# Kernel optimization log

Measured on AMD Instinct MI355X. Metric: run time of the kernel, lower is better.

The kernel has to match this reference:

```python
import jax, jax.numpy as jnp
import numpy as np

N_NODES = 50000
N_EDGES = 800000
NEG_SLOPE = 0.2  # PyG GATv2Conv default
EPS = 1e-16      # PyG softmax denominator epsilon


def _segment_softmax(logits, seg, num_segments):
    # logits: [E, H]; seg: [E] target-node ids
    m = jax.ops.segment_max(logits, seg, num_segments=num_segments)
    p = jnp.exp(logits - m[seg])
    s = jax.ops.segment_sum(p, seg, num_segments=num_segments)
    return p / (s[seg] + EPS)


def _gatv2_conv(x, src, dst, Wl, Wr, att, bias, heads, out_ch, concat):
    # x: [N, F]; Wl/Wr: [F, heads*out_ch]; att: [heads, out_ch]
    n = x.shape[0]
    xl = (x @ Wl).reshape(n, heads, out_ch)
    xr = (x @ Wr).reshape(n, heads, out_ch)
    # GATv2: e_ij = att . leaky_relu(xl[j] + xr[i]) for edge j->i
    e = jax.nn.leaky_relu(xl[src] + xr[dst], NEG_SLOPE)  # [E, H, C]
    logit = jnp.einsum('ehc,hc->eh', e, att)             # [E, H]
    alpha = _segment_softmax(logit, dst, n)              # [E, H]
    out = jax.ops.segment_sum(alpha[:, :, None] * xl[src], dst, num_segments=n)  # [N, H, C]
    if concat:
        out = out.reshape(n, heads * out_ch)
    else:
        out = out.mean(axis=1)
    return out + bias


def setup_inputs() -> dict:
    key = jax.random.key(0)
    ks = jax.random.split(key, 20)
    in_ch, hid, out_ch, heads, edge_dim = 128, 128, 64, 8, 6
    c1 = hid // heads  # 16
    g = lambda k, shp, fan: (jax.random.normal(k, shp, jnp.float32) / np.sqrt(fan)).astype(jnp.float32)
    inp = {
        'x': jax.random.normal(ks[0], (N_NODES, in_ch), jnp.float32),
        'edge_index': jax.random.randint(ks[1], (2, N_EDGES), 0, N_NODES, dtype=jnp.int64),
        'edge_attr': jax.random.normal(ks[2], (N_EDGES, edge_dim), jnp.float32),
        'Wl1': g(ks[3], (in_ch, heads * c1), in_ch),
        'Wr1': g(ks[4], (in_ch, heads * c1), in_ch),
        'att1': g(ks[5], (heads, c1), c1),
        'b1': jnp.zeros((heads * c1,), jnp.float32),
        # layer 2: GATv2Conv(hid -> out_ch, heads=1, no concat)
        'Wl2': g(ks[6], (hid, out_ch), hid),
        'Wr2': g(ks[7], (hid, out_ch), hid),
        'att2': g(ks[8], (1, out_ch), out_ch),
        'b2': jnp.zeros((out_ch,), jnp.float32),
        # edge encoder (computed but unused downstream, as in the source)
        'We1': g(ks[9], (edge_dim, hid), edge_dim), 'be1': jnp.zeros((hid,), jnp.float32),
        'We2': g(ks[10], (hid, hid), hid), 'be2': jnp.zeros((hid,), jnp.float32),
        # classifier
        'Wc1': g(ks[11], (out_ch, hid), out_ch), 'bc1': jnp.zeros((hid,), jnp.float32),
        'Wc2': g(ks[12], (hid, 2), hid), 'bc2': jnp.zeros((2,), jnp.float32),
    }
    return inp


def reference(x, edge_index, edge_attr, Wl1, Wr1, att1, b1, Wl2, Wr2, att2, b2,
              We1, be1, We2, be2, Wc1, bc1, Wc2, bc2):
    n = x.shape[0]
    # edge encoder (dead code in the original forward; kept for fidelity)
    _edge_feats = jax.nn.relu(edge_attr @ We1 + be1) @ We2 + be2
    # add self-loops (PyG GATv2Conv default add_self_loops=True)
    loop = jnp.arange(n, dtype=edge_index.dtype)
    src = jnp.concatenate([edge_index[0], loop])
    dst = jnp.concatenate([edge_index[1], loop])
    # layer 1 (heads=8, concat) + relu; dropout is identity in eval
    h = _gatv2_conv(x, src, dst, Wl1, Wr1, att1, b1, heads=8, out_ch=16, concat=True)
    h = jax.nn.relu(h)
    # layer 2 (heads=1, mean)
    emb = _gatv2_conv(h, src, dst, Wl2, Wr2, att2, b2, heads=1, out_ch=64, concat=False)
    logits = jax.nn.relu(emb @ Wc1 + bc1) @ Wc2 + bc2
    return emb, logits
```

## Files before the change

kernel.cpp:

```cpp
#include <hip/hip_runtime.h>
#include <hip/hip_bf16.h>
#include <cfloat>

#define N_NODES 50000
#define N_EDGES 800000
#define E_TOT   850000
#define NEG_SLOPE 0.2f
#define SM_EPS 1e-16f
#define SCAN_B 196
#define LOG2E 1.4426950408889634f

typedef __attribute__((ext_vector_type(8))) short short8;
typedef __attribute__((ext_vector_type(4))) float f32x4;

__device__ __forceinline__ float lrelu(float v) { return v > 0.0f ? v : NEG_SLOPE * v; }

__device__ __forceinline__ unsigned f2bf_pack2(float a, float b) {
    unsigned ua = __float_as_uint(a);
    ua += 0x7fff + ((ua >> 16) & 1);
    unsigned ub = __float_as_uint(b);
    ub += 0x7fff + ((ub >> 16) & 1);
    return (ua >> 16) | (ub & 0xffff0000u);
}
__device__ __forceinline__ unsigned short f2bf(float a) {
    unsigned ua = __float_as_uint(a);
    ua += 0x7fff + ((ua >> 16) & 1);
    return (unsigned short)(ua >> 16);
}
__device__ __forceinline__ float bf_lo(unsigned u) { return __uint_as_float(u << 16); }
__device__ __forceinline__ float bf_hi(unsigned u) { return __uint_as_float(u & 0xffff0000u); }

__device__ __forceinline__ unsigned short pack_one(const float* __restrict__ B0,
                                                   const float* __restrict__ B1,
                                                   int i, int N) {
    int m   = i / (128 * N);
    int rem = i % (128 * N);
    int j    = rem & 7;
    int quad = (rem >> 3) & 3;
    int n    = (rem >> 5) & 15;
    int ctk  = rem >> 9;
    int ct   = ctk % (N / 16);
    int kt   = ctk / (N / 16);
    int k    = kt * 32 + quad * 8 + j;
    int col  = ct * 16 + n;
    const float* B = m ? B1 : B0;
    return f2bf(B[k * N + col]);
}

__global__ void prep(const float* __restrict__ Wl1, const float* __restrict__ Wr1,
                     const float* __restrict__ Wl2, const float* __restrict__ Wr2,
                     const float* __restrict__ Wc1,
                     unsigned short* __restrict__ Bp1, unsigned short* __restrict__ Bp2,
                     unsigned short* __restrict__ Wc1p,
                     int* __restrict__ flags) {
    int i = blockIdx.x * 256 + threadIdx.x;
    if (i < 32768) {
        Bp1[i] = pack_one(Wl1, Wr1, i, 128);
    } else if (i < 49152) {
        Bp2[i - 32768] = pack_one(Wl2, Wr2, i - 32768, 64);
    } else if (i < 57344) {
        int idx = i - 49152;
        int j    = idx & 7;
        int quad = (idx >> 3) & 3;
        int n    = (idx >> 5) & 15;
        int ctk  = idx >> 9;
        int ct   = ctk & 7;
        int kt   = ctk >> 3;
        Wc1p[idx] = f2bf(Wc1[(kt * 32 + quad * 8 + j) * 128 + ct * 16 + n]);
    } else if (i < 57600) {
        flags[i - 57344] = 0;
    }
}

__device__ __forceinline__ void gemm128_both(int b, const float* __restrict__ x,
                                             const unsigned short* __restrict__ Bp1,
                                             unsigned short* __restrict__ xlbf,
                                             float* __restrict__ xr1, int M) {
    int w = threadIdx.x >> 6, lane = threadIdx.x & 63;
    int quad = lane >> 4, l16 = lane & 15;
    int row0 = b * 32 + (w & 1) * 16;
    int cb   = (w >> 1) * 64;
    f32x4 accL[4], accR[4];
    #pragma unroll
    for (int t = 0; t < 4; ++t) {
        accL[t] = (f32x4){0.f, 0.f, 0.f, 0.f};
        accR[t] = (f32x4){0.f, 0.f, 0.f, 0.f};
    }
    int arow = row0 + l16;
    bool aok = arow < M;
    #pragma unroll
    for (int kt = 0; kt < 4; ++kt) {
        short8 a = (short8)0;
        if (aok) {
            const float* Ap = x + (size_t)arow * 128 + quad * 8 + kt * 32;
            float4 f0 = *(const float4*)(Ap);
            float4 f1 = *(const float4*)(Ap + 4);
            union { uint4 u; short8 s; } cv;
            cv.u.x = f2bf_pack2(f0.x, f0.y);
            cv.u.y = f2bf_pack2(f0.z, f0.w);
            cv.u.z = f2bf_pack2(f1.x, f1.y);
            cv.u.w = f2bf_pack2(f1.z, f1.w);
            a = cv.s;
        }
        #pragma unroll
        for (int t = 0; t < 4; ++t) {
            int ct = (cb >> 4) + t;
            const short* bp = (const short*)Bp1 + (((kt * 8 + ct) * 16 + l16) * 4 + quad) * 8;
            short8 bL = *(const short8*)bp;
            short8 bR = *(const short8*)(bp + 128 * 128);
            accL[t] = __builtin_amdgcn_mfma_f32_16x16x32_bf16(a, bL, accL[t], 0, 0, 0);
            accR[t] = __builtin_amdgcn_mfma_f32_16x16x32_bf16(a, bR, accR[t], 0, 0, 0);
        }
    }
    #pragma unroll
    for (int t = 0; t < 4; ++t) {
        int col = cb + t * 16 + l16;
        #pragma unroll
        for (int r = 0; r < 4; ++r) {
            int row = row0 + quad * 4 + r;
            if (row < M) {
                xlbf[(size_t)row * 128 + col] = f2bf(accL[t][r]);
                xr1[(size_t)row * 128 + col]  = accR[t][r];
            }
        }
    }
}

__global__ __launch_bounds__(256)
void k2_count_gemms(const int* __restrict__ ei, unsigned* __restrict__ deg8,
                    unsigned short* __restrict__ rank16,
                    const float* __restrict__ x, const unsigned short* __restrict__ Bp1,
                    unsigned short* __restrict__ xlbf, float* __restrict__ xr1, int M) {
    int b = blockIdx.x;
    int c = b / 3, rem = b % 3;
    if (rem == 2) {
        int nz = __syncthreads_or(ei[2 * threadIdx.x + 1]);
        int i = c * 256 + threadIdx.x;
        if (4 * i >= N_EDGES) return;
        int d0, d1, d2, d3;
        if (nz) {
            int4 dp = *(const int4*)(ei + N_EDGES + 4 * i);
            d0 = dp.x; d1 = dp.y; d2 = dp.z; d3 = dp.w;
        } else {
            int4 a0 = *(const int4*)(ei + 2 * N_EDGES + 8 * i);
            int4 a1 = *(const int4*)(ei + 2 * N_EDGES + 8 * i + 4);
            d0 = a0.x; d1 = a0.z; d2 = a1.x; d3 = a1.z;
        }
        unsigned xcd;
        asm volatile("s_getreg_b32 %0, hwreg(HW_REG_XCC_ID)" : "=s"(xcd));
        xcd &= 7u;
        unsigned* dg = deg8 + xcd * 50000u;
        unsigned tag = xcd << 13;
        unsigned r0 = __hip_atomic_fetch_add(&dg[d0], 1u, __ATOMIC_RELAXED, __HIP_MEMORY_SCOPE_WORKGROUP);
        unsigned r1 = __hip_atomic_fetch_add(&dg[d1], 1u, __ATOMIC_RELAXED, __HIP_MEMORY_SCOPE_WORKGROUP);
        unsigned r2 = __hip_atomic_fetch_add(&dg[d2], 1u, __ATOMIC_RELAXED, __HIP_MEMORY_SCOPE_WORKGROUP);
        unsigned r3 = __hip_atomic_fetch_add(&dg[d3], 1u, __ATOMIC_RELAXED, __HIP_MEMORY_SCOPE_WORKGROUP);
        uint2 pk;
        pk.x = (r0 | tag) | ((r1 | tag) << 16);
        pk.y = (r2 | tag) | ((r3 | tag) << 16);
        *(uint2*)(rank16 + 4 * i) = pk;
    } else {
        int g = 2 * c + rem;
        if (g >= 1563) return;
        gemm128_both(g, x, Bp1, xlbf, xr1, M);
    }
}

__global__ void scan_fused(const unsigned* __restrict__ deg8, int* __restrict__ rowptr,
                           int* __restrict__ esrc, int* __restrict__ bsum,
                           int* __restrict__ flags, int* __restrict__ base8) {
    __shared__ int sh[256];
    int b = blockIdx.x, t = threadIdx.x, i = b * 256 + t;
    unsigned d[8];
    int tot = 0;
    if (i < N_NODES) {
        #pragma unroll
        for (int xk = 0; xk < 8; ++xk) { d[xk] = deg8[xk * 50000 + i]; tot += (int)d[xk]; }
    }
    int v = (i < N_NODES) ? tot + 1 : 0;
    sh[t] = v;
    __syncthreads();
    int val = v;
    for (int off = 1; off < 256; off <<= 1) {
        int add = (t >= off) ? sh[t - off] : 0;
        __syncthreads();
        val += add; sh[t] = val;
        __syncthreads();
    }
    if (t == 255) {
        bsum[b] = val;
        __threadfence();
        atomicExch(&flags[b], 1);
    }
    int contrib = 0;
    if (t < b) {
        while (atomicAdd(&flags[t], 0) == 0) {}
        contrib = atomicAdd(&bsum[t], 0);
    }
    __syncthreads();
    sh[t] = contrib;
    __syncthreads();
    #pragma unroll
    for (int off = 128; off; off >>= 1) {
        if (t < off) sh[t] += sh[t + off];
        __syncthreads();
    }
    int offset = sh[0];
    if (i < N_NODES) {
        int rp = (val - v) + offset;
        rowptr[i] = rp;
        esrc[rp] = i;
        int acc = rp + 1;
        #pragma unroll
        for (int xk = 0; xk < 8; ++xk) { base8[xk * 50000 + i] = acc; acc += (int)d[xk]; }
    }
    if (i == 0) rowptr[N_NODES] = E_TOT;
}

__global__ void scatter_edges(const int* __restrict__ ei, const int* __restrict__ base8,
                              const unsigned short* __restrict__ rank16,
                              int* __restrict__ esrc) {
    int nz = __syncthreads_or(ei[2 * threadIdx.x + 1]);
    int i = blockIdx.x * blockDim.x + threadIdx.x;
    if (2 * i >= N_EDGES) return;
    bool has2 = (2 * i + 1 < N_EDGES);
    int s0, d0, s1 = 0, d1 = 0;
    if (nz) {
        int2 sp = *(const int2*)(ei + 2 * i);
        int2 dp = *(const int2*)(ei + N_EDGES + 2 * i);
        s0 = sp.x; s1 = sp.y; d0 = dp.x; d1 = dp.y;
    } else {
        int4 sp = *(const int4*)(ei + 4 * i);
        int4 dp = *(const int4*)(ei + 2 * N_EDGES + 4 * i);
        s0 = sp.x; s1 = sp.z; d0 = dp.x; d1 = dp.z;
    }
    unsigned rr = *(const unsigned*)(rank16 + 2 * i);
    unsigned r0 = rr & 0xffffu, r1 = rr >> 16;
    esrc[base8[(r0 >> 13) * 50000 + d0] + (int)(r0 & 0x1fffu)] = s0;
    if (has2) esrc[base8[(r1 >> 13) * 50000 + d1] + (int)(r1 & 0x1fffu)] = s1;
}

__global__ __launch_bounds__(256)
void gemm_mfma64(const unsigned short* __restrict__ Abf, const unsigned short* __restrict__ Bp,
                 unsigned short* __restrict__ C0bf, float* __restrict__ C1, int M) {
    int w = threadIdx.x >> 6, lane = threadIdx.x & 63;
    int quad = lane >> 4, l16 = lane & 15;
    int matrix = w >> 1;
    int row0 = blockIdx.x * 32 + (w & 1) * 16;
    const unsigned short* Bm = Bp + matrix * 128 * 64;
    f32x4 acc[4];
    #pragma unroll
    for (int t = 0; t < 4; ++t) acc[t] = (f32x4){0.f, 0.f, 0.f, 0.f};
    int arow = row0 + l16;
    bool aok = arow < M;
    const short* Ap = (const short*)Abf + (size_t)arow * 128 + quad * 8;
    #pragma unroll
    for (int kt = 0; kt < 4; ++kt) {
        short8 a = (short8)0;
        if (aok) a = *(const short8*)(Ap + kt * 32);
        #pragma unroll
        for (int t = 0; t < 4; ++t) {
            const short* bp = (const short*)Bm + (((kt * 4 + t) * 16 + l16) * 4 + quad) * 8;
            short8 bfr = *(const short8*)bp;
            acc[t] = __builtin_amdgcn_mfma_f32_16x16x32_bf16(a, bfr, acc[t], 0, 0, 0);
        }
    }
    #pragma unroll
    for (int t = 0; t < 4; ++t) {
        int col = t * 16 + l16;
        #pragma unroll
        for (int r = 0; r < 4; ++r) {
            int row = row0 + quad * 4 + r;
            if (row < M) {
                if (matrix) C1[(size_t)row * 64 + col] = acc[t][r];
                else        C0bf[(size_t)row * 64 + col] = f2bf(acc[t][r]);
            }
        }
    }
}

__global__ __launch_bounds__(256)
void node_fused1(const int* __restrict__ rowptr, const int* __restrict__ esrc,
                 const unsigned short* __restrict__ xlbf, const float* __restrict__ xr,
                 const float* __restrict__ att, const float* __restrict__ b1,
                 unsigned short* __restrict__ hbf) {
    int wave = threadIdx.x >> 6;
    int lane = threadIdx.x & 63;
    int n = blockIdx.x * 4 + wave;
    int slot = lane >> 4;
    int l = lane & 15;
    int beg = rowptr[n], end = rowptr[n + 1];
    const float* xrp = xr + (size_t)n * 128 + 8 * l;
    float4 xra = *(const float4*)(xrp);
    float4 xrb = *(const float4*)(xrp + 4);
    float4 ata = *(const float4*)(att + 8 * l);
    float4 atb = *(const float4*)(att + 8 * l + 4);
    ata.x *= LOG2E; ata.y *= LOG2E; ata.z *= LOG2E; ata.w *= LOG2E;
    atb.x *= LOG2E; atb.y *= LOG2E; atb.z *= LOG2E; atb.w *= LOG2E;
    float den = 0.0f;
    float4 aa = {0, 0, 0, 0}, ab = {0, 0, 0, 0};

    auto body = [&](int k) {
        int s = esrc[k];
        uint4 u = *(const uint4*)(xlbf + (size_t)s * 128 + 8 * l);
        float x0 = bf_lo(u.x), x1 = bf_hi(u.x);
        float x2 = bf_lo(u.y), x3 = bf_hi(u.y);
        float x4 = bf_lo(u.z), x5 = bf_hi(u.z);
        float x6 = bf_lo(u.w), x7 = bf_hi(u.w);
        float v = ata.x * lrelu(x0 + xra.x) + ata.y * lrelu(x1 + xra.y)
                + ata.z * lrelu(x2 + xra.z) + ata.w * lrelu(x3 + xra.w)
                + atb.x * lrelu(x4 + xrb.x) + atb.y * lrelu(x5 + xrb.y)
                + atb.z * lrelu(x6 + xrb.z) + atb.w * lrelu(x7 + xrb.w);
        v += __shfl_xor(v, 1);
        float p = exp2f(v);
        den += p;
        aa.x += p * x0; aa.y += p * x1; aa.z += p * x2; aa.w += p * x3;
        ab.x += p * x4; ab.y += p * x5; ab.z += p * x6; ab.w += p * x7;
    };
    int k = beg + slot;
    for (; k + 4 < end; k += 8) { body(k); body(k + 4); }
    if (k < end) body(k);

    #pragma unroll
    for (int off = 16; off < 64; off <<= 1) {
        aa.x += __shfl_xor(aa.x, off); aa.y += __shfl_xor(aa.y, off);
        aa.z += __shfl_xor(aa.z, off); aa.w += __shfl_xor(aa.w, off);
        ab.x += __shfl_xor(ab.x, off); ab.y += __shfl_xor(ab.y, off);
        ab.z += __shfl_xor(ab.z, off); ab.w += __shfl_xor(ab.w, off);
        den   += __shfl_xor(den, off);
    }
    if (slot == 0) {
        float inv = 1.0f / (den + SM_EPS);
        float4 b4a = *(const float4*)(b1 + 8 * l);
        float4 b4b = *(const float4*)(b1 + 8 * l + 4);
        float oa0 = fmaxf(aa.x * inv + b4a.x, 0.0f);
        float oa1 = fmaxf(aa.y * inv + b4a.y, 0.0f);
        float oa2 = fmaxf(aa.z * inv + b4a.z, 0.0f);
        float oa3 = fmaxf(aa.w * inv + b4a.w, 0.0f);
        float ob0 = fmaxf(ab.x * inv + b4b.x, 0.0f);
        float ob1 = fmaxf(ab.y * inv + b4b.y, 0.0f);
        float ob2 = fmaxf(ab.z * inv + b4b.z, 0.0f);
        float ob3 = fmaxf(ab.w * inv + b4b.w, 0.0f);
        uint4 pk;
        pk.x = f2bf_pack2(oa0, oa1);
        pk.y = f2bf_pack2(oa2, oa3);
        pk.z = f2bf_pack2(ob0, ob1);
        pk.w = f2bf_pack2(ob2, ob3);
        *(uint4*)(hbf + (size_t)n * 128 + 8 * l) = pk;
    }
}

__global__ __launch_bounds__(256)
void node_fused2(const int* __restrict__ rowptr, const int* __restrict__ esrc,
                 const unsigned short* __restrict__ xlbf, const float* __restrict__ xr,
                 const float* __restrict__ att, const float* __restrict__ b2v,
                 float* __restrict__ out_emb, unsigned short* __restrict__ embbf) {
    int wave = threadIdx.x >> 6;
    int lane = threadIdx.x & 63;
    int n = blockIdx.x * 4 + wave;
    int slot = lane >> 3;
    int l = lane & 7;
    int beg = rowptr[n], end = rowptr[n + 1];
    const float* xrp = xr + (size_t)n * 64 + 8 * l;
    float4 xra = *(const float4*)(xrp);
    float4 xrb = *(const float4*)(xrp + 4);
    float4 ata = *(const float4*)(att + 8 * l);
    float4 atb = *(const float4*)(att + 8 * l + 4);
    ata.x *= LOG2E; ata.y *= LOG2E; ata.z *= LOG2E; ata.w *= LOG2E;
    atb.x *= LOG2E; atb.y *= LOG2E; atb.z *= LOG2E; atb.w *= LOG2E;
    float den = 0.0f;
    float4 aa = {0, 0, 0, 0}, ab = {0, 0, 0, 0};

    auto body = [&](int k) {
        int s = esrc[k];
        uint4 u = *(const uint4*)(xlbf + (size_t)s * 64 + 8 * l);
        float x0 = bf_lo(u.x), x1 = bf_hi(u.x);
        float x2 = bf_lo(u.y), x3 = bf_hi(u.y);
        float x4 = bf_lo(u.z), x5 = bf_hi(u.z);
        float x6 = bf_lo(u.w), x7 = bf_hi(u.w);
        float v = ata.x * lrelu(x0 + xra.x) + ata.y * lrelu(x1 + xra.y)
                + ata.z * lrelu(x2 + xra.z) + ata.w * lrelu(x3 + xra.w)
                + atb.x * lrelu(x4 + xrb.x) + atb.y * lrelu(x5 + xrb.y)
                + atb.z * lrelu(x6 + xrb.z) + atb.w * lrelu(x7 + xrb.w);
        v += __shfl_xor(v, 1);
        v += __shfl_xor(v, 2);
        v += __shfl_xor(v, 4);
        float p = exp2f(v);
        den += p;
        aa.x += p * x0; aa.y += p * x1; aa.z += p * x2; aa.w += p * x3;
        ab.x += p * x4; ab.y += p * x5; ab.z += p * x6; ab.w += p * x7;
    };
    int k = beg + slot;
    for (; k + 8 < end; k += 16) { body(k); body(k + 8); }
    if (k < end) body(k);

    #pragma unroll
    for (int off = 8; off < 64; off <<= 1) {
        aa.x += __shfl_xor(aa.x, off); aa.y += __shfl_xor(aa.y, off);
        aa.z += __shfl_xor(aa.z, off); aa.w += __shfl_xor(aa.w, off);
        ab.x += __shfl_xor(ab.x, off); ab.y += __shfl_xor(ab.y, off);
        ab.z += __shfl_xor(ab.z, off); ab.w += __shfl_xor(ab.w, off);
        den   += __shfl_xor(den, off);
    }
    if (slot == 0) {
        float inv = 1.0f / (den + SM_EPS);
        float4 b4a = *(const float4*)(b2v + 8 * l);
        float4 b4b = *(const float4*)(b2v + 8 * l + 4);
        float4 ea, eb;
        ea.x = aa.x * inv + b4a.x; ea.y = aa.y * inv + b4a.y;
        ea.z = aa.z * inv + b4a.z; ea.w = aa.w * inv + b4a.w;
        eb.x = ab.x * inv + b4b.x; eb.y = ab.y * inv + b4b.y;
        eb.z = ab.z * inv + b4b.z; eb.w = ab.w * inv + b4b.w;
        float* op = out_emb + (size_t)n * 64 + 8 * l;
        *(float4*)(op)     = ea;
        *(float4*)(op + 4) = eb;
        uint4 pk;
        pk.x = f2bf_pack2(ea.x, ea.y);
        pk.y = f2bf_pack2(ea.z, ea.w);
        pk.z = f2bf_pack2(eb.x, eb.y);
        pk.w = f2bf_pack2(eb.z, eb.w);
        *(uint4*)(embbf + (size_t)n * 64 + 8 * l) = pk;
    }
}

__global__ __launch_bounds__(256)
void cls_mfma(const unsigned short* __restrict__ embbf, const unsigned short* __restrict__ Wc1p,
              const float* __restrict__ bc1, const float* __restrict__ Wc2,
              const float* __restrict__ bc2, float* __restrict__ out_logits) {
    __shared__ float part[2][16][2][2];
    int w = threadIdx.x >> 6, lane = threadIdx.x & 63;
    int quad = lane >> 4, l16 = lane & 15;
    int rowhalf = w & 1, colhalf = w >> 1;
    int row0 = blockIdx.x * 32 + rowhalf * 16;
    int cb = colhalf * 64;
    f32x4 acc[4];
    #pragma unroll
    for (int t = 0; t < 4; ++t) acc[t] = (f32x4){0.f, 0.f, 0.f, 0.f};
    int arow = row0 + l16;
    bool aok = arow < N_NODES;
    const short* Ap = (const short*)embbf + (size_t)arow * 64 + quad * 8;
    #pragma unroll
    for (int kt = 0; kt < 2; ++kt) {
        short8 a = (short8)0;
        if (aok) a = *(const short8*)(Ap + kt * 32);
        #pragma unroll
        for (int t = 0; t < 4; ++t) {
            int ct = colhalf * 4 + t;
            const short* bp = (const short*)Wc1p + (((kt * 8 + ct) * 16 + l16) * 4 + quad) * 8;
            short8 bfr = *(const short8*)bp;
            acc[t] = __builtin_amdgcn_mfma_f32_16x16x32_bf16(a, bfr, acc[t], 0, 0, 0);
        }
    }
    float p0[4] = {0, 0, 0, 0}, p1[4] = {0, 0, 0, 0};
    #pragma unroll
    for (int t = 0; t < 4; ++t) {
        int col = cb + t * 16 + l16;
        float w2a = Wc2[2 * col], w2b = Wc2[2 * col + 1];
        float bc = bc1[col];
        #pragma unroll
        for (int r = 0; r < 4; ++r) {
            float tv = fmaxf(acc[t][r] + bc, 0.0f);
            p0[r] += tv * w2a;
            p1[r] += tv * w2b;
        }
    }
    #pragma unroll
    for (int off = 1; off < 16; off <<= 1) {
        #pragma unroll
        for (int r = 0; r < 4; ++r) {
            p0[r] += __shfl_xor(p0[r], off);
            p1[r] += __shfl_xor(p1[r], off);
        }
    }
    if (l16 == 0) {
        #pragma unroll
        for (int r = 0; r < 4; ++r) {
            part[rowhalf][quad * 4 + r][colhalf][0] = p0[r];
            part[rowhalf][quad * 4 + r][colhalf][1] = p1[r];
        }
    }
    __syncthreads();
    int t = threadIdx.x;
    if (t < 64) {
        int row = t >> 1, c = t & 1;
        int rh = row >> 4, r16 = row & 15;
        float s = part[rh][r16][0][c] + part[rh][r16][1][c] + bc2[c];
        int n = blockIdx.x * 32 + row;
        if (n < N_NODES) out_logits[(size_t)n * 2 + c] = s;
    }
}

extern "C" void kernel_launch(void* const* d_in, const int* in_sizes, int n_in,
                              void* d_out, int out_size, void* d_ws, size_t ws_size,
                              hipStream_t stream) {
    const float* x    = (const float*)d_in[0];
    const int*   ei   = (const int*)d_in[1];
    const float* Wl1  = (const float*)d_in[3];
    const float* Wr1  = (const float*)d_in[4];
    const float* att1 = (const float*)d_in[5];
    const float* b1   = (const float*)d_in[6];
    const float* Wl2  = (const float*)d_in[7];
    const float* Wr2  = (const float*)d_in[8];
    const float* att2 = (const float*)d_in[9];
    const float* b2   = (const float*)d_in[10];
    const float* Wc1  = (const float*)d_in[15];
    const float* bc1  = (const float*)d_in[16];
    const float* Wc2  = (const float*)d_in[17];
    const float* bc2  = (const float*)d_in[18];

    float* ws = (float*)d_ws;
    int* rowptr = (int*)ws + 50000;
    int* esrc   = rowptr + 50016;
    int* bsum   = esrc + 850000;
    int* flags  = bsum + 256;
    unsigned short* rank16 = (unsigned short*)(flags + 256);
    float* xr1           = ws + 1400448;
    unsigned short* xlbf = (unsigned short*)(ws + 7800448);
    unsigned short* hbf  = (unsigned short*)(ws + 11000448);
    unsigned* deg8 = (unsigned*)(ws + 11000448);
    int* base8     = (int*)(ws + 11400448);
    unsigned short* Bp1   = (unsigned short*)(ws + 14200448);
    unsigned short* Bp2   = (unsigned short*)(ws + 14216832);
    unsigned short* Wc1p  = (unsigned short*)(ws + 14225024);
    unsigned short* embbf = (unsigned short*)(ws + 14229120);

    float* out_emb    = (float*)d_out;
    float* out_logits = out_emb + (size_t)N_NODES * 64;

    hipMemsetAsync(deg8, 0, 400000 * sizeof(unsigned), stream);

    prep<<<225, 256, 0, stream>>>(Wl1, Wr1, Wl2, Wr2, Wc1, Bp1, Bp2, Wc1p, flags);

    k2_count_gemms<<<2346, 256, 0, stream>>>(ei, deg8, rank16, x, Bp1, xlbf, xr1, N_NODES);

    scan_fused<<<SCAN_B, 256, 0, stream>>>(deg8, rowptr, esrc, bsum, flags, base8);

    scatter_edges<<<1563, 256, 0, stream>>>(ei, base8, rank16, esrc);

    node_fused1<<<12500, 256, 0, stream>>>(rowptr, esrc, xlbf, xr1, att1, b1, hbf);

    gemm_mfma64<<<1563, 256, 0, stream>>>(hbf, Bp2, xlbf, xr1, N_NODES);
    node_fused2<<<12500, 256, 0, stream>>>(rowptr, esrc, xlbf, xr1, att2, b2, out_emb, embbf);

    cls_mfma<<<1563, 256, 0, stream>>>(embbf, Wc1p, bc1, Wc2, bc2, out_logits);
}
```

Baseline: 296.2 us.

## Replace global per-XCD degree atomics with LDS-privatized chunked histograms

Degree counting now uses 256 blocks, each covering one of 8 node ranges and one of 32 edge chunks. Each block counts into a shared-memory histogram with LDS atomics and writes a per-(range,chunk) histogram, which removes the global atomics and the memset of the degree array. The scan and scatter kernels are changed to read and write the larger 32-way per-chunk base array. Every counting block now reads its whole edge chunk (an 8x redundant read of the destination indices), and the scan does 32 strided loads and stores per node.

```diff
diff --git a/kernel.cpp b/kernel.cpp
--- a/kernel.cpp
+++ b/kernel.cpp
@@ -9,6 +9,11 @@
 #define SM_EPS 1e-16f
 #define SCAN_B 196
 #define LOG2E 1.4426950408889634f
+
+#define NCH 32
+#define CSZ 25000
+#define NR  8
+#define RSZ 6250
 
 typedef __attribute__((ext_vector_type(8))) short short8;
 typedef __attribute__((ext_vector_type(4))) float f32x4;
@@ -127,55 +132,57 @@
 }
 
 __global__ __launch_bounds__(256)
-void k2_count_gemms(const int* __restrict__ ei, unsigned* __restrict__ deg8,
+void k2_count_gemms(const int* __restrict__ ei, unsigned* __restrict__ hist,
                     unsigned short* __restrict__ rank16,
                     const float* __restrict__ x, const unsigned short* __restrict__ Bp1,
                     unsigned short* __restrict__ xlbf, float* __restrict__ xr1, int M) {
+    __shared__ unsigned hcnt[RSZ];
     int b = blockIdx.x;
-    int c = b / 3, rem = b % 3;
-    if (rem == 2) {
+    if (b < NR * NCH) {
+        int r = b >> 5, c = b & 31;
+        for (int i = threadIdx.x; i < RSZ; i += 256) hcnt[i] = 0;
         int nz = __syncthreads_or(ei[2 * threadIdx.x + 1]);
-        int i = c * 256 + threadIdx.x;
-        if (4 * i >= N_EDGES) return;
-        int d0, d1, d2, d3;
-        if (nz) {
-            int4 dp = *(const int4*)(ei + N_EDGES + 4 * i);
-            d0 = dp.x; d1 = dp.y; d2 = dp.z; d3 = dp.w;
-        } else {
-            int4 a0 = *(const int4*)(ei + 2 * N_EDGES + 8 * i);
-            int4 a1 = *(const int4*)(ei + 2 * N_EDGES + 8 * i + 4);
-            d0 = a0.x; d1 = a0.z; d2 = a1.x; d3 = a1.z;
-        }
-        unsigned xcd;
-        asm volatile("s_getreg_b32 %0, hwreg(HW_REG_XCC_ID)" : "=s"(xcd));
-        xcd &= 7u;
-        unsigned* dg = deg8 + xcd * 50000u;
-        unsigned tag = xcd << 13;
-        unsigned r0 = __hip_atomic_fetch_add(&dg[d0], 1u, __ATOMIC_RELAXED, __HIP_MEMORY_SCOPE_WORKGROUP);
-        unsigned r1 = __hip_atomic_fetch_add(&dg[d1], 1u, __ATOMIC_RELAXED, __HIP_MEMORY_SCOPE_WORKGROUP);
-        unsigned r2 = __hip_atomic_fetch_add(&dg[d2], 1u, __ATOMIC_RELAXED, __HIP_MEMORY_SCOPE_WORKGROUP);
-        unsigned r3 = __hip_atomic_fetch_add(&dg[d3], 1u, __ATOMIC_RELAXED, __HIP_MEMORY_SCOPE_WORKGROUP);
-        uint2 pk;
-        pk.x = (r0 | tag) | ((r1 | tag) << 16);
-        pk.y = (r2 | tag) | ((r3 | tag) << 16);
-        *(uint2*)(rank16 + 4 * i) = pk;
+        int nlo = r * RSZ, nhi = nlo + RSZ;
+        int cbeg = c * CSZ, cend = cbeg + CSZ;
+        for (int e = cbeg + (int)threadIdx.x; e < cend; e += 1024) {
+            int dd[4];
+            #pragma unroll
+            for (int j = 0; j < 4; ++j) {
+                int ee = e + j * 256;
+                dd[j] = -1;
+                if (ee < cend)
+                    dd[j] = nz ? ei[N_EDGES + ee] : ei[2 * N_EDGES + 2 * ee];
+            }
+            #pragma unroll
+            for (int j = 0; j < 4; ++j) {
+                int d = dd[j];
+                if (d >= nlo && d < nhi) {
+                    unsigned rk = atomicAdd(&hcnt[d - nlo], 1u);
+                    rank16[e + j * 256] = (unsigned short)rk;
+                }
+            }
+        }
+        __syncthreads();
+        unsigned* hp = hist + (size_t)(r * NCH + c) * RSZ;
+        for (int i = threadIdx.x; i < RSZ; i += 256) hp[i] = hcnt[i];
     } else {
-        int g = 2 * c + rem;
-        if (g >= 1563) return;
-        gemm128_both(g, x, Bp1, xlbf, xr1, M);
-    }
-}
-
-__global__ void scan_fused(const unsigned* __restrict__ deg8, int* __restrict__ rowptr,
+        gemm128_both(b - NR * NCH, x, Bp1, xlbf, xr1, M);
+    }
+}
+
+__global__ void scan_fused(const unsigned* __restrict__ hist, int* __restrict__ rowptr,
                            int* __restrict__ esrc, int* __restrict__ bsum,
-                           int* __restrict__ flags, int* __restrict__ base8) {
+                           int* __restrict__ flags, int* __restrict__ base) {
     __shared__ int sh[256];
     int b = blockIdx.x, t = threadIdx.x, i = b * 256 + t;
-    unsigned d[8];
+    unsigned d[NCH];
     int tot = 0;
+    int rr = 0, q = 0;
     if (i < N_NODES) {
-        #pragma unroll
-        for (int xk = 0; xk < 8; ++xk) { d[xk] = deg8[xk * 50000 + i]; tot += (int)d[xk]; }
+        rr = i / RSZ; q = i - rr * RSZ;
+        const unsigned* hp = hist + (size_t)rr * NCH * RSZ + q;
+        #pragma unroll
+        for (int c = 0; c < NCH; ++c) { d[c] = hp[(size_t)c * RSZ]; tot += (int)d[c]; }
     }
     int v = (i < N_NODES) ? tot + 1 : 0;
     sh[t] = v;
@@ -211,13 +218,14 @@
         rowptr[i] = rp;
         esrc[rp] = i;
         int acc = rp + 1;
-        #pragma unroll
-        for (int xk = 0; xk < 8; ++xk) { base8[xk * 50000 + i] = acc; acc += (int)d[xk]; }
+        int* bp = base + (size_t)rr * NCH * RSZ + q;
+        #pragma unroll
+        for (int c = 0; c < NCH; ++c) { bp[(size_t)c * RSZ] = acc; acc += (int)d[c]; }
     }
     if (i == 0) rowptr[N_NODES] = E_TOT;
 }
 
-__global__ void scatter_edges(const int* __restrict__ ei, const int* __restrict__ base8,
+__global__ void scatter_edges(const int* __restrict__ ei, const int* __restrict__ base,
                               const unsigned short* __restrict__ rank16,
                               int* __restrict__ esrc) {
     int nz = __syncthreads_or(ei[2 * threadIdx.x + 1]);
@@ -235,9 +243,12 @@
         s0 = sp.x; s1 = sp.z; d0 = dp.x; d1 = dp.z;
     }
     unsigned rr = *(const unsigned*)(rank16 + 2 * i);
-    unsigned r0 = rr & 0xffffu, r1 = rr >> 16;
-    esrc[base8[(r0 >> 13) * 50000 + d0] + (int)(r0 & 0x1fffu)] = s0;
-    if (has2) esrc[base8[(r1 >> 13) * 50000 + d1] + (int)(r1 & 0x1fffu)] = s1;
+    int e0 = 2 * i, e1 = 2 * i + 1;
+    int c0 = e0 / CSZ, c1 = e1 / CSZ;
+    int r0 = d0 / RSZ, r1 = d1 / RSZ;
+    esrc[base[((size_t)r0 * NCH + c0) * RSZ + (d0 - r0 * RSZ)] + (int)(rr & 0xffffu)] = s0;
+    if (has2)
+        esrc[base[((size_t)r1 * NCH + c1) * RSZ + (d1 - r1 * RSZ)] + (int)(rr >> 16)] = s1;
 }
 
 __global__ __launch_bounds__(256)
@@ -517,8 +528,8 @@
     float* xr1           = ws + 1400448;
     unsigned short* xlbf = (unsigned short*)(ws + 7800448);
     unsigned short* hbf  = (unsigned short*)(ws + 11000448);
-    unsigned* deg8 = (unsigned*)(ws + 11000448);
-    int* base8     = (int*)(ws + 11400448);
+    unsigned* hist = (unsigned*)(ws + 11000448);
+    int* base      = (int*)(ws + 12600448);
     unsigned short* Bp1   = (unsigned short*)(ws + 14200448);
     unsigned short* Bp2   = (unsigned short*)(ws + 14216832);
     unsigned short* Wc1p  = (unsigned short*)(ws + 14225024);
@@ -527,15 +538,13 @@
     float* out_emb    = (float*)d_out;
     float* out_logits = out_emb + (size_t)N_NODES * 64;
 
-    hipMemsetAsync(deg8, 0, 400000 * sizeof(unsigned), stream);
-
     prep<<<225, 256, 0, stream>>>(Wl1, Wr1, Wl2, Wr2, Wc1, Bp1, Bp2, Wc1p, flags);
 
-    k2_count_gemms<<<2346, 256, 0, stream>>>(ei, deg8, rank16, x, Bp1, xlbf, xr1, N_NODES);
-
-    scan_fused<<<SCAN_B, 256, 0, stream>>>(deg8, rowptr, esrc, bsum, flags, base8);
-
-    scatter_edges<<<1563, 256, 0, stream>>>(ei, base8, rank16, esrc);
+    k2_count_gemms<<<256 + 1563, 256, 0, stream>>>(ei, hist, rank16, x, Bp1, xlbf, xr1, N_NODES);
+
+    scan_fused<<<SCAN_B, 256, 0, stream>>>(hist, rowptr, esrc, bsum, flags, base);
+
+    scatter_edges<<<1563, 256, 0, stream>>>(ei, base, rank16, esrc);
 
     node_fused1<<<12500, 256, 0, stream>>>(rowptr, esrc, xlbf, xr1, att1, b1, hbf);
 
```

After: 287.0 us. -3.1%, faster.
